# Optimization experiments

Hardware: AMD Instinct MI355X
Metric: run time of the kernel (lower is better)

The kernel has to match this reference:

```python
import jax, jax.numpy as jnp
import numpy as np


def setup_inputs() -> dict:
    key = jax.random.key(0)
    k1, k2, k3, k4 = jax.random.split(key, 4)
    B, S, D, Y = 8, 2048, 512, 8921
    # xavier_uniform scale for [Y, D] weights
    lim = float(np.sqrt(6.0 / (Y + D)))
    x = jax.random.normal(k1, (B, S, D), dtype=jnp.float32)
    U_w = jax.random.uniform(k2, (Y, D), minval=-lim, maxval=lim, dtype=jnp.float32)
    final_w = jax.random.uniform(k3, (Y, D), minval=-lim, maxval=lim, dtype=jnp.float32)
    final_b = jax.random.normal(k4, (Y,), dtype=jnp.float32) * 0.02
    return {"x": x, "U_w": U_w, "final_w": final_w, "final_b": final_b}


def reference(x, U_w, final_w, final_b):
    # att: [B, Y, S] = U_w @ x^T
    att = jnp.einsum("yd,bsd->bys", U_w, x)
    alpha = jax.nn.softmax(att, axis=2)          # softmax over sequence
    m = jnp.einsum("bys,bsd->byd", alpha, x)      # per-label context [B, Y, D]
    y = jnp.einsum("yd,byd->by", final_w, m) + final_b  # [B, Y]
    return y
```

## Files before the change

### kernel.cpp

```cpp
#include <hip/hip_runtime.h>
#include <hip/hip_bf16.h>

constexpr int B_ = 8;
constexpr int S_ = 2048;
constexpr int D_ = 512;
constexpr int Y_ = 8921;
constexpr int MT_ = 140;
constexpr int SG_ = 8;

typedef __attribute__((ext_vector_type(8))) __bf16 bf16x8;
typedef __attribute__((ext_vector_type(4))) float f32x4;

__device__ __forceinline__ int swz32(int row, int ksel) {
  return row * 32 + (((ksel ^ (row >> 1)) & 3) << 3);
}

__global__ __launch_bounds__(256) void cvtW(const float* __restrict__ U,
                                            const float* __restrict__ F,
                                            __hip_bfloat16* __restrict__ wsW) {
  const int c = blockIdx.x * 256 + threadIdx.x;
  const int tile = c >> 9;
  const int row = (c >> 2) & 127;
  const int cs = c & 3;
  const int mt = tile >> 4, kt = tile & 15;
  const int ch = (cs ^ (row >> 1)) & 3;
  const int g = row >> 5, h = (row >> 4) & 1, w = row & 15;
  const int y = mt * 64 + g * 16 + w;
  float4 f0 = {0.f, 0.f, 0.f, 0.f}, f1 = {0.f, 0.f, 0.f, 0.f};
  if (y < Y_) {
    const float* src = (h ? F : U) + (size_t)y * D_ + kt * 32 + ch * 8;
    f0 = reinterpret_cast<const float4*>(src)[0];
    f1 = reinterpret_cast<const float4*>(src)[1];
  }
  bf16x8 v;
  v[0] = (__bf16)f0.x; v[1] = (__bf16)f0.y; v[2] = (__bf16)f0.z; v[3] = (__bf16)f0.w;
  v[4] = (__bf16)f1.x; v[5] = (__bf16)f1.y; v[6] = (__bf16)f1.z; v[7] = (__bf16)f1.w;
  *reinterpret_cast<bf16x8*>(wsW + (size_t)c * 8) = v;
}

__global__ __launch_bounds__(256) void cvtX(const float* __restrict__ x,
                                            __hip_bfloat16* __restrict__ wsX) {
  const int c = blockIdx.x * 256 + threadIdx.x;
  const int tile = c >> 10;
  const int row = (c >> 2) & 255;
  const int cs = c & 3;
  const int b = tile >> 7, st = (tile >> 4) & 7, kt = tile & 15;
  const int ch = (cs ^ (row >> 1)) & 3;
  const int s = st * 256 + row;
  const float* src = x + ((size_t)b * S_ + s) * D_ + kt * 32 + ch * 8;
  const float4 f0 = reinterpret_cast<const float4*>(src)[0];
  const float4 f1 = reinterpret_cast<const float4*>(src)[1];
  bf16x8 v;
  v[0] = (__bf16)f0.x; v[1] = (__bf16)f0.y; v[2] = (__bf16)f0.z; v[3] = (__bf16)f0.w;
  v[4] = (__bf16)f1.x; v[5] = (__bf16)f1.y; v[6] = (__bf16)f1.z; v[7] = (__bf16)f1.w;
  *reinterpret_cast<bf16x8*>(wsX + (size_t)c * 8) = v;
}

__global__ __launch_bounds__(256) void zeroLN(float* __restrict__ LN, int n) {
  const int i = blockIdx.x * 256 + threadIdx.x;
  if (i < n) LN[i] = 0.f;
}

__global__ __launch_bounds__(256) void combine(const float* __restrict__ Lg,
                                               const float* __restrict__ Ng,
                                               const float* __restrict__ fb,
                                               float* __restrict__ out) {
  const int y = blockIdx.x * 256 + threadIdx.x;
  const int b = blockIdx.y;
  if (y < Y_) out[(size_t)b * Y_ + y] = Ng[b * Y_ + y] / Lg[b * Y_ + y] + fb[y];
}

typedef const __attribute__((address_space(1))) void gv_t;
typedef __attribute__((address_space(3))) void lv_t;

__device__ __forceinline__ void gld_lds16(const void* g, void* l) {
  __builtin_amdgcn_global_load_lds((gv_t*)g, (lv_t*)l, 16, 0, 0);
}

__global__ __launch_bounds__(512, 4) void pool_main(
    const __hip_bfloat16* __restrict__ wsW, const __hip_bfloat16* __restrict__ wsX,
    float* __restrict__ Lg, float* __restrict__ Ng) {
  const int bid = blockIdx.x;
  const int b = bid & 7;
  const int r = bid >> 3;
  const int mt = r % MT_;
  const int sg = r / MT_;

  const int tid = threadIdx.x;
  const int lane = tid & 63;
  const int wid = tid >> 6;
  const int wm = wid >> 2;
  const int wn = wid & 3;
  const int l15 = lane & 15;
  const int l4 = lane >> 4;

  __shared__ __bf16 sW[3][4096];
  __shared__ __bf16 sX[3][8192];
  __shared__ float red[128];

  if (tid < 128) red[tid] = 0.f;

  const __bf16* Wbase = (const __bf16*)wsW + (size_t)mt * 16 * 4096;
  const __bf16* Xbase = (const __bf16*)wsX + (size_t)((b * 8 + sg) * 16) * 8192;

  f32x4 acc[4][4];
#pragma unroll
  for (int m = 0; m < 4; ++m)
#pragma unroll
    for (int n = 0; n < 4; ++n) acc[m][n] = (f32x4){0.f, 0.f, 0.f, 0.f};

  auto stageBoth = [&](int t1, int buf) {
    const char* srcW = (const char*)(Wbase + t1 * 4096) + tid * 16;
    const char* srcX = (const char*)(Xbase + (size_t)t1 * 8192) + tid * 16;
    gld_lds16(srcW, (char*)sW[buf] + tid * 16);
    gld_lds16(srcX, (char*)sX[buf] + tid * 16);
    gld_lds16(srcX + 8192, (char*)sX[buf] + 8192 + tid * 16);
  };

  stageBoth(0, 0);
  stageBoth(1, 1);

  int cur = 0;
  int nx2 = 2;

  for (int t = 0; t < 16; ++t) {
    if (t < 15) asm volatile("s_waitcnt vmcnt(3)" ::: "memory");
    else        asm volatile("s_waitcnt vmcnt(0)" ::: "memory");
    __builtin_amdgcn_s_barrier();
    __builtin_amdgcn_sched_barrier(0);

    if (t < 14) stageBoth(t + 2, nx2);

    const __bf16* A = sW[cur];
    const __bf16* Xl = sX[cur];

    bf16x8 af[4], xf[4];
#pragma unroll
    for (int j = 0; j < 4; ++j)
      af[j] = *reinterpret_cast<const bf16x8*>(&A[swz32(wm * 64 + j * 16 + l15, l4)]);
#pragma unroll
    for (int n = 0; n < 4; ++n)
      xf[n] = *reinterpret_cast<const bf16x8*>(&Xl[swz32(wn * 64 + n * 16 + l15, l4)]);
    __builtin_amdgcn_s_setprio(1);
#pragma unroll
    for (int j = 0; j < 4; ++j)
#pragma unroll
      for (int n = 0; n < 4; ++n)
        acc[j][n] = __builtin_amdgcn_mfma_f32_16x16x32_bf16(af[j], xf[n], acc[j][n], 0, 0, 0);
    __builtin_amdgcn_s_setprio(0);
    __builtin_amdgcn_sched_barrier(0);

    cur = (cur == 2) ? 0 : cur + 1;
    nx2 = (nx2 == 2) ? 0 : nx2 + 1;
  }

#pragma unroll
  for (int g = 0; g < 2; ++g)
#pragma unroll
    for (int q = 0; q < 4; ++q) {
      float l = 0.f, nn = 0.f;
#pragma unroll
      for (int n = 0; n < 4; ++n) {
        const float e = __expf(acc[2 * g][n][q]);
        l += e;
        nn = fmaf(e, acc[2 * g + 1][n][q], nn);
      }
#pragma unroll
      for (int mask = 1; mask <= 8; mask <<= 1) {
        l += __shfl_xor(l, mask);
        nn += __shfl_xor(nn, mask);
      }
      if (l15 == 0) {
        const int yl = wm * 32 + g * 16 + (l4 << 2) + q;
        atomicAdd(&red[yl], l);
        atomicAdd(&red[64 + yl], nn);
      }
    }

  __syncthreads();
  if (tid < 64) {
    const int y = mt * 64 + tid;
    if (y < Y_) {
      atomicAdd(&Lg[(size_t)b * Y_ + y], red[tid]);
      atomicAdd(&Ng[(size_t)b * Y_ + y], red[64 + tid]);
    }
  }
}

constexpr int FB_BY = 128, FB_BS = 64, FB_BK = 64;

__device__ __forceinline__ int fswz(int row, int k) {
  return row * FB_BK + ((((k >> 3) ^ row) & 7) << 3) + (k & 7);
}

template <int CHUNKS>
__device__ __forceinline__ void fb_stage(const float* __restrict__ gbase, int rstride,
                                         int maxrow, __bf16* lds, int tid) {
#pragma unroll
  for (int i = 0; i < CHUNKS / 256; ++i) {
    const int c = tid + 256 * i;
    const int row = c >> 3;
    const int ch = c & 7;
    float4 f0 = {0.f, 0.f, 0.f, 0.f}, f1 = {0.f, 0.f, 0.f, 0.f};
    if (row < maxrow) {
      const float4* p = reinterpret_cast<const float4*>(gbase + (size_t)row * rstride + ch * 8);
      f0 = p[0]; f1 = p[1];
    }
    bf16x8 v;
    v[0] = (__bf16)f0.x; v[1] = (__bf16)f0.y; v[2] = (__bf16)f0.z; v[3] = (__bf16)f0.w;
    v[4] = (__bf16)f1.x; v[5] = (__bf16)f1.y; v[6] = (__bf16)f1.z; v[7] = (__bf16)f1.w;
    *reinterpret_cast<bf16x8*>(&lds[fswz(row, ch * 8)]) = v;
  }
}

__global__ __launch_bounds__(256) void output_layer_fallback(
    const float* __restrict__ x, const float* __restrict__ Uw,
    const float* __restrict__ Fw, const float* __restrict__ fb,
    float* __restrict__ out) {
  const int b = blockIdx.y;
  const int y0 = blockIdx.x * FB_BY;
  const int tid = threadIdx.x;
  const int lane = tid & 63;
  const int w = tid >> 6;
  const int wm = (w >> 1) * 64, wn = (w & 1) * 32;
  __shared__ __bf16 sU[FB_BY * FB_BK], sF[FB_BY * FB_BK], sX[FB_BS * FB_BK];
  float Ls[4][4], Ns[4][4];
#pragma unroll
  for (int m = 0; m < 4; ++m)
#pragma unroll
    for (int q = 0; q < 4; ++q) { Ls[m][q] = 0.f; Ns[m][q] = 0.f; }
  const float* xb = x + (size_t)b * S_ * D_;
  const int umax = Y_ - y0;
  for (int s0 = 0; s0 < S_; s0 += FB_BS) {
    f32x4 accA[4][2] = {}, accP[4][2] = {};
    for (int k0 = 0; k0 < D_; k0 += FB_BK) {
      __syncthreads();
      fb_stage<FB_BY * 8>(Uw + (size_t)y0 * D_ + k0, D_, umax, sU, tid);
      fb_stage<FB_BY * 8>(Fw + (size_t)y0 * D_ + k0, D_, umax, sF, tid);
      fb_stage<FB_BS * 8>(xb + (size_t)s0 * D_ + k0, D_, FB_BS, sX, tid);
      __syncthreads();
#pragma unroll
      for (int kk = 0; kk < 2; ++kk) {
        const int kb = kk * 32 + (lane >> 4) * 8;
        bf16x8 bx[2];
#pragma unroll
        for (int n = 0; n < 2; ++n)
          bx[n] = *reinterpret_cast<const bf16x8*>(&sX[fswz(wn + n * 16 + (lane & 15), kb)]);
#pragma unroll
        for (int m = 0; m < 4; ++m) {
          const bf16x8 aU = *reinterpret_cast<const bf16x8*>(&sU[fswz(wm + m * 16 + (lane & 15), kb)]);
          const bf16x8 aF = *reinterpret_cast<const bf16x8*>(&sF[fswz(wm + m * 16 + (lane & 15), kb)]);
#pragma unroll
          for (int n = 0; n < 2; ++n) {
            accA[m][n] = __builtin_amdgcn_mfma_f32_16x16x32_bf16(aU, bx[n], accA[m][n], 0, 0, 0);
            accP[m][n] = __builtin_amdgcn_mfma_f32_16x16x32_bf16(aF, bx[n], accP[m][n], 0, 0, 0);
          }
        }
      }
    }
#pragma unroll
    for (int m = 0; m < 4; ++m)
#pragma unroll
      for (int n = 0; n < 2; ++n)
#pragma unroll
        for (int q = 0; q < 4; ++q) {
          const float e = __expf(accA[m][n][q]);
          Ls[m][q] += e;
          Ns[m][q] = fmaf(e, accP[m][n][q], Ns[m][q]);
        }
  }
  __syncthreads();
  float* redL = reinterpret_cast<float*>(sU);
  float* redN = reinterpret_cast<float*>(sF);
  for (int i = tid; i < FB_BY; i += 256) { redL[i] = 0.f; redN[i] = 0.f; }
  __syncthreads();
#pragma unroll
  for (int m = 0; m < 4; ++m)
#pragma unroll
    for (int q = 0; q < 4; ++q) {
      float l = Ls[m][q], nn = Ns[m][q];
#pragma unroll
      for (int mask = 1; mask <= 8; mask <<= 1) {
        l += __shfl_xor(l, mask);
        nn += __shfl_xor(nn, mask);
      }
      if ((lane & 15) == 0) {
        const int yl = wm + m * 16 + ((lane >> 4) << 2) + q;
        atomicAdd(&redL[yl], l);
        atomicAdd(&redN[yl], nn);
      }
    }
  __syncthreads();
  for (int i = tid; i < FB_BY; i += 256) {
    const int y = y0 + i;
    if (y < Y_) out[(size_t)b * Y_ + y] = redN[i] / redL[i] + fb[y];
  }
}

extern "C" void kernel_launch(void* const* d_in, const int* in_sizes, int n_in,
                              void* d_out, int out_size, void* d_ws,
                              size_t ws_size, hipStream_t stream) {
  const float* x = (const float*)d_in[0];
  const float* Uw = (const float*)d_in[1];
  const float* Fw = (const float*)d_in[2];
  const float* fb = (const float*)d_in[3];
  float* out = (float*)d_out;

  constexpr size_t W_EL = (size_t)MT_ * 16 * 4096;
  constexpr size_t X_EL = (size_t)B_ * 8 * 16 * 8192;
  constexpr size_t LN_FL = (size_t)2 * B_ * Y_;
  constexpr size_t WS_NEED = (W_EL + X_EL) * 2 + LN_FL * 4;

  if (ws_size >= WS_NEED) {
    __hip_bfloat16* wsW = (__hip_bfloat16*)d_ws;
    __hip_bfloat16* wsX = wsW + W_EL;
    float* Lg = (float*)(wsX + X_EL);
    float* Ng = Lg + (size_t)B_ * Y_;

    cvtW<<<dim3((unsigned)(W_EL / 8 / 256)), dim3(256), 0, stream>>>(Uw, Fw, wsW);
    cvtX<<<dim3((unsigned)(X_EL / 8 / 256)), dim3(256), 0, stream>>>(x, wsX);
    zeroLN<<<dim3((unsigned)((LN_FL + 255) / 256)), dim3(256), 0, stream>>>(Lg, (int)LN_FL);

    pool_main<<<dim3(MT_ * B_ * SG_), dim3(512), 0, stream>>>(wsW, wsX, Lg, Ng);
    combine<<<dim3((Y_ + 255) / 256, B_), dim3(256), 0, stream>>>(Lg, Ng, fb, out);
  } else {
    output_layer_fallback<<<dim3(MT_ / 2 + 5, B_), dim3(256), 0, stream>>>(x, Uw, Fw, fb, out);
  }
}
```

Baseline: 344.8 us.

## Load X fragments directly into registers instead of staging through LDS

The X conversion kernel now writes bf16 data in a per-wave MFMA fragment order, so the main kernel can load each wave's X operands straight from global memory into registers with double-buffered register sets. This removes the X LDS buffers and their async copies, leaving only W staged through LDS, and cuts LDS traffic and shared memory use. The launch bound is lowered to two blocks per SM to give room for the extra registers. The cost is more register pressure, possible lower occupancy, and global-load latency exposed directly on the MFMA path.

```diff
diff --git a/kernel.cpp b/kernel.cpp
--- a/kernel.cpp
+++ b/kernel.cpp
@@ -41,13 +41,15 @@
 __global__ __launch_bounds__(256) void cvtX(const float* __restrict__ x,
                                             __hip_bfloat16* __restrict__ wsX) {
   const int c = blockIdx.x * 256 + threadIdx.x;
-  const int tile = c >> 10;
-  const int row = (c >> 2) & 255;
-  const int cs = c & 3;
-  const int b = tile >> 7, st = (tile >> 4) & 7, kt = tile & 15;
-  const int ch = (cs ^ (row >> 1)) & 3;
-  const int s = st * 256 + row;
-  const float* src = x + ((size_t)b * S_ + s) * D_ + kt * 32 + ch * 8;
+  const int lane = c & 63;
+  const int n = (c >> 6) & 3;
+  const int wn = (c >> 8) & 3;
+  const int kt = (c >> 10) & 15;
+  const int st = (c >> 14) & 7;
+  const int b = (c >> 17) & 7;
+  const int s = st * 256 + wn * 64 + n * 16 + (lane & 15);
+  const int k = kt * 32 + (lane >> 4) * 8;
+  const float* src = x + ((size_t)b * S_ + s) * D_ + k;
   const float4 f0 = reinterpret_cast<const float4*>(src)[0];
   const float4 f1 = reinterpret_cast<const float4*>(src)[1];
   bf16x8 v;
@@ -77,7 +79,7 @@
   __builtin_amdgcn_global_load_lds((gv_t*)g, (lv_t*)l, 16, 0, 0);
 }
 
-__global__ __launch_bounds__(512, 4) void pool_main(
+__global__ __launch_bounds__(512, 2) void pool_main(
     const __hip_bfloat16* __restrict__ wsW, const __hip_bfloat16* __restrict__ wsX,
     float* __restrict__ Lg, float* __restrict__ Ng) {
   const int bid = blockIdx.x;
@@ -95,13 +97,13 @@
   const int l4 = lane >> 4;
 
   __shared__ __bf16 sW[3][4096];
-  __shared__ __bf16 sX[3][8192];
   __shared__ float red[128];
 
   if (tid < 128) red[tid] = 0.f;
 
   const __bf16* Wbase = (const __bf16*)wsW + (size_t)mt * 16 * 4096;
-  const __bf16* Xbase = (const __bf16*)wsX + (size_t)((b * 8 + sg) * 16) * 8192;
+  const __bf16* Xw = (const __bf16*)wsX +
+      (size_t)((b * 8 + sg) * 16) * 8192 + wn * 2048 + lane * 8;
 
   f32x4 acc[4][4];
 #pragma unroll
@@ -109,50 +111,73 @@
 #pragma unroll
     for (int n = 0; n < 4; ++n) acc[m][n] = (f32x4){0.f, 0.f, 0.f, 0.f};
 
-  auto stageBoth = [&](int t1, int buf) {
-    const char* srcW = (const char*)(Wbase + t1 * 4096) + tid * 16;
-    const char* srcX = (const char*)(Xbase + (size_t)t1 * 8192) + tid * 16;
-    gld_lds16(srcW, (char*)sW[buf] + tid * 16);
-    gld_lds16(srcX, (char*)sX[buf] + tid * 16);
-    gld_lds16(srcX + 8192, (char*)sX[buf] + 8192 + tid * 16);
+  auto stageW = [&](int t1, int buf) {
+    gld_lds16((const char*)(Wbase + t1 * 4096) + tid * 16,
+              (char*)sW[buf] + tid * 16);
   };
 
-  stageBoth(0, 0);
-  stageBoth(1, 1);
-
+  bf16x8 xfP[4], xfQ[4];
+
+  stageW(0, 0);
+#pragma unroll
+  for (int n = 0; n < 4; ++n)
+    xfP[n] = *reinterpret_cast<const bf16x8*>(Xw + n * 512);
+  __builtin_amdgcn_sched_barrier(0);
+  stageW(1, 1);
+#pragma unroll
+  for (int n = 0; n < 4; ++n)
+    xfQ[n] = *reinterpret_cast<const bf16x8*>(Xw + 8192 + n * 512);
+  __builtin_amdgcn_sched_barrier(0);
+
+  const __bf16* xc2 = Xw + 2 * 8192;
   int cur = 0;
   int nx2 = 2;
 
-  for (int t = 0; t < 16; ++t) {
-    if (t < 15) asm volatile("s_waitcnt vmcnt(3)" ::: "memory");
-    else        asm volatile("s_waitcnt vmcnt(0)" ::: "memory");
-    __builtin_amdgcn_s_barrier();
-    __builtin_amdgcn_sched_barrier(0);
-
-    if (t < 14) stageBoth(t + 2, nx2);
-
-    const __bf16* A = sW[cur];
-    const __bf16* Xl = sX[cur];
-
-    bf16x8 af[4], xf[4];
-#pragma unroll
-    for (int j = 0; j < 4; ++j)
-      af[j] = *reinterpret_cast<const bf16x8*>(&A[swz32(wm * 64 + j * 16 + l15, l4)]);
-#pragma unroll
-    for (int n = 0; n < 4; ++n)
-      xf[n] = *reinterpret_cast<const bf16x8*>(&Xl[swz32(wn * 64 + n * 16 + l15, l4)]);
-    __builtin_amdgcn_s_setprio(1);
-#pragma unroll
-    for (int j = 0; j < 4; ++j)
-#pragma unroll
-      for (int n = 0; n < 4; ++n)
-        acc[j][n] = __builtin_amdgcn_mfma_f32_16x16x32_bf16(af[j], xf[n], acc[j][n], 0, 0, 0);
-    __builtin_amdgcn_s_setprio(0);
-    __builtin_amdgcn_sched_barrier(0);
-
-    cur = (cur == 2) ? 0 : cur + 1;
-    nx2 = (nx2 == 2) ? 0 : nx2 + 1;
-  }
+#define STEP(XF, PRE, LAST)                                                    \
+  {                                                                            \
+    if (LAST) asm volatile("s_waitcnt vmcnt(0)" ::: "memory");                 \
+    else      asm volatile("s_waitcnt vmcnt(5)" ::: "memory");                 \
+    __builtin_amdgcn_s_barrier();                                              \
+    __builtin_amdgcn_sched_barrier(0);                                         \
+    if (PRE) stageW(tW, nx2);                                                  \
+    bf16x8 af[4];                                                              \
+    _Pragma("unroll")                                                          \
+    for (int j = 0; j < 4; ++j)                                                \
+      af[j] = *reinterpret_cast<const bf16x8*>(                                \
+          &sW[cur][swz32(wm * 64 + j * 16 + l15, l4)]);                        \
+    __builtin_amdgcn_s_setprio(1);                                             \
+    _Pragma("unroll")                                                          \
+    for (int j = 0; j < 4; ++j)                                                \
+      _Pragma("unroll")                                                        \
+      for (int n = 0; n < 4; ++n)                                              \
+        acc[j][n] = __builtin_amdgcn_mfma_f32_16x16x32_bf16(af[j], XF[n],      \
+                                                            acc[j][n], 0, 0, 0);\
+    __builtin_amdgcn_s_setprio(0);                                             \
+    if (PRE) {                                                                 \
+      _Pragma("unroll")                                                        \
+      for (int n = 0; n < 4; ++n)                                              \
+        XF[n] = *reinterpret_cast<const bf16x8*>(xc2 + n * 512);               \
+      xc2 += 8192;                                                             \
+    }                                                                          \
+    __builtin_amdgcn_sched_barrier(0);                                         \
+    cur = (cur == 2) ? 0 : cur + 1;                                            \
+    nx2 = (nx2 == 2) ? 0 : nx2 + 1;                                            \
+  }
+
+  for (int it = 0; it < 8; ++it) {
+    const bool pre = (it < 7);
+    {
+      const int tW = 2 * it + 2;
+      STEP(xfP, pre, false)
+    }
+    {
+      const int tW = 2 * it + 3;
+      STEP(xfQ, pre, (it == 7))
+    }
+    if (it == 3) {
+    }
+  }
+#undef STEP
 
 #pragma unroll
   for (int g = 0; g < 2; ++g)
```

Result: slower. 420.4 us (+21.9%).
